# Kernel tuning notes

Hardware: AMD Instinct MI355X
Metric: run time of the kernel (lower is better)

The kernel has to match this reference:

```python
import jax, jax.numpy as jnp
import numpy as np

HIDDEN = 1024
N_HEADS = 16
N_LAYERS = 10
LOCAL_K = 3
TOKEN_T, TOKEN_H, TOKEN_W = 4, 16, 16
PATCH_SIZE = 2
LATENT_C = 16
TOKEN_DIM = LATENT_C * PATCH_SIZE * PATCH_SIZE  # 64
TOKEN_IN = TOKEN_DIM + 1                        # 65
N_TOKENS = TOKEN_T * TOKEN_H * TOKEN_W          # 1024
B = 1
HEAD_DIM = HIDDEN // N_HEADS
LN_EPS = 1e-5


def layer_norm(x, w, b):
    m = x.mean(-1, keepdims=True)
    v = ((x - m) ** 2).mean(-1, keepdims=True)
    return (x - m) * jax.lax.rsqrt(v + LN_EPS) * w + b


def patchify(lat):
    Bx, T, C, H, W = lat.shape
    ph, pw = H // PATCH_SIZE, W // PATCH_SIZE
    x = lat.reshape(Bx, T, C, ph, PATCH_SIZE, pw, PATCH_SIZE)
    x = x.transpose(0, 1, 3, 5, 2, 4, 6)
    return x.reshape(Bx, T * ph * pw, C * PATCH_SIZE * PATCH_SIZE)


def unpatchify(tok):
    Bx = tok.shape[0]
    C = TOKEN_DIM // (PATCH_SIZE * PATCH_SIZE)
    x = tok.reshape(Bx, TOKEN_T, TOKEN_H, TOKEN_W, C, PATCH_SIZE, PATCH_SIZE)
    x = x.transpose(0, 1, 4, 2, 5, 3, 6)
    return x.reshape(Bx, TOKEN_T, C, TOKEN_H * PATCH_SIZE, TOKEN_W * PATCH_SIZE)


def gather_neighbors(kv):
    # kv: (B, N, 2D) -> (B, N, 27, 2D), 3x3x3 zero-padded neighborhoods
    Bx, Nx, D2 = kv.shape
    pad = LOCAL_K // 2
    x = kv.reshape(Bx, TOKEN_T, TOKEN_H, TOKEN_W, D2)
    x = jnp.pad(x, ((0, 0), (pad, pad), (pad, pad), (pad, pad), (0, 0)))
    sl = [x[:, dt:dt + TOKEN_T, dh:dh + TOKEN_H, dw:dw + TOKEN_W]
          for dt in range(LOCAL_K) for dh in range(LOCAL_K) for dw in range(LOCAL_K)]
    nb = jnp.stack(sl, axis=4)  # (B,T,H,W,27,2D)
    return nb.reshape(Bx, Nx, LOCAL_K ** 3, D2)


def local_attention(x, qkv_w, out_w):
    Bx, Nx, D = x.shape
    H, d = N_HEADS, HEAD_DIM
    qkv = x @ qkv_w                       # (B,N,3D)
    q, k, v = jnp.split(qkv, 3, axis=-1)
    kv_nb = gather_neighbors(jnp.concatenate([k, v], axis=-1))  # (B,N,27,2D)
    k_nb, v_nb = jnp.split(kv_nb, 2, axis=-1)
    q = q.reshape(Bx, Nx, H, d)
    k_nb = k_nb.reshape(Bx, Nx, LOCAL_K ** 3, H, d)
    v_nb = v_nb.reshape(Bx, Nx, LOCAL_K ** 3, H, d)
    scores = jnp.einsum('bnhd,bnkhd->bnhk', q, k_nb) / np.sqrt(d).astype(np.float32)
    probs = jax.nn.softmax(scores, axis=-1)
    out = jnp.einsum('bnhk,bnkhd->bnhd', probs, v_nb).reshape(Bx, Nx, D)
    return out @ out_w


def global_attention(x, mask_flat, qkv_w, out_w):
    # Each masked query attends to all N keys; math identical to the
    # gather/SDPA/scatter in the original (per-query attention is independent),
    # realized as full attention masked to zero at unmasked positions.
    Bx, Nx, D = x.shape
    H, d = N_HEADS, HEAD_DIM
    qkv = x @ qkv_w
    q, k, v = jnp.split(qkv, 3, axis=-1)
    q = q.reshape(Bx, Nx, H, d)
    k = k.reshape(Bx, Nx, H, d)
    v = v.reshape(Bx, Nx, H, d)
    scores = jnp.einsum('bqhd,bkhd->bhqk', q, k) / np.sqrt(d).astype(np.float32)
    probs = jax.nn.softmax(scores, axis=-1)
    out = jnp.einsum('bhqk,bkhd->bqhd', probs, v).reshape(Bx, Nx, D)
    out = out @ out_w
    return out * mask_flat[..., None].astype(out.dtype)


def setup_inputs() -> dict:
    key = jax.random.key(0)
    ks = jax.random.split(key, 24)
    s = 0.02
    L, D = N_LAYERS, HIDDEN
    inp = {
        'latents': jax.random.normal(ks[0], (B, TOKEN_T, LATENT_C, TOKEN_H * PATCH_SIZE, TOKEN_W * PATCH_SIZE), jnp.float32),
        'token_mask': jax.random.uniform(ks[1], (B, TOKEN_T, TOKEN_H, TOKEN_W)) < 0.1,
        'input_proj_w': jax.random.normal(ks[2], (TOKEN_IN, D), jnp.float32) * s,
        'input_proj_b': jnp.zeros((D,), jnp.float32),
        'emb_t': jax.random.normal(ks[3], (TOKEN_T, D), jnp.float32) * s,
        'emb_h': jax.random.normal(ks[4], (TOKEN_H, D), jnp.float32) * s,
        'emb_w': jax.random.normal(ks[5], (TOKEN_W, D), jnp.float32) * s,
        'ln_local_w': jnp.ones((L, D), jnp.float32),
        'ln_local_b': jnp.zeros((L, D), jnp.float32),
        'ln_global_w': jnp.ones((L, D), jnp.float32),
        'ln_global_b': jnp.zeros((L, D), jnp.float32),
        'ln_ffn_w': jnp.ones((L, D), jnp.float32),
        'ln_ffn_b': jnp.zeros((L, D), jnp.float32),
        'local_qkv_w': jax.random.normal(ks[6], (L, D, 3 * D), jnp.float32) * s,
        'local_out_w': jax.random.normal(ks[7], (L, D, D), jnp.float32) * s,
        'global_qkv_w': jax.random.normal(ks[8], (L, D, 3 * D), jnp.float32) * s,
        'global_out_w': jax.random.normal(ks[9], (L, D, D), jnp.float32) * s,
        'ffn_w1': jax.random.normal(ks[10], (L, D, 4 * D), jnp.float32) * s,
        'ffn_b1': jnp.zeros((L, 4 * D), jnp.float32),
        'ffn_w2': jax.random.normal(ks[11], (L, 4 * D, D), jnp.float32) * s,
        'ffn_b2': jnp.zeros((L, D), jnp.float32),
        'final_ln_w': jnp.ones((D,), jnp.float32),
        'final_ln_b': jnp.zeros((D,), jnp.float32),
        # original zero-inits output_proj; use small random so the test is non-trivial
        'out_proj_w': jax.random.normal(ks[12], (D, TOKEN_DIM), jnp.float32) * s,
        'out_proj_b': jnp.zeros((TOKEN_DIM,), jnp.float32),
    }
    return inp


def reference(latents, token_mask, input_proj_w, input_proj_b, emb_t, emb_h, emb_w,
              ln_local_w, ln_local_b, ln_global_w, ln_global_b, ln_ffn_w, ln_ffn_b,
              local_qkv_w, local_out_w, global_qkv_w, global_out_w,
              ffn_w1, ffn_b1, ffn_w2, ffn_b2, final_ln_w, final_ln_b,
              out_proj_w, out_proj_b):
    Bx = latents.shape[0]
    mask_flat = token_mask.reshape(Bx, -1)
    tokens = patchify(latents)                       # (B, N, TOKEN_DIM)
    flag = mask_flat[..., None].astype(tokens.dtype)
    x = jnp.concatenate([tokens, flag], axis=-1) @ input_proj_w + input_proj_b

    tt, hh, ww = jnp.meshgrid(jnp.arange(TOKEN_T), jnp.arange(TOKEN_H), jnp.arange(TOKEN_W), indexing='ij')
    pos = emb_t[tt.reshape(-1)] + emb_h[hh.reshape(-1)] + emb_w[ww.reshape(-1)]
    x = x + pos[None]

    for l in range(N_LAYERS):
        x = x + local_attention(layer_norm(x, ln_local_w[l], ln_local_b[l]), local_qkv_w[l], local_out_w[l])
        x = x + global_attention(layer_norm(x, ln_global_w[l], ln_global_b[l]), mask_flat, global_qkv_w[l], global_out_w[l])
        h = layer_norm(x, ln_ffn_w[l], ln_ffn_b[l])
        h = jax.nn.gelu(h @ ffn_w1[l] + ffn_b1[l], approximate=False) @ ffn_w2[l] + ffn_b2[l]
        x = x + h

    delta = layer_norm(x, final_ln_w, final_ln_b) @ out_proj_w + out_proj_b
    return unpatchify(tokens + delta)
```

## Files before the change

kernel.cpp:

```cpp
#include <hip/hip_runtime.h>
#include <hip/hip_bf16.h>
#include <math.h>

typedef __bf16 bf16;
typedef __bf16 bf16x8 __attribute__((ext_vector_type(8)));
typedef __bf16 bf16x4 __attribute__((ext_vector_type(4)));
typedef float  f32x4 __attribute__((ext_vector_type(4)));
typedef unsigned int u32x4 __attribute__((ext_vector_type(4)));

#define NTOK 1024
#define HID  1024
#define NL   10
#define QCMAX 256

#define EPI_F32   0
#define EPI_GELU  1
#define EPI_RESID 2
#define EPI_BF16  3

__global__ __launch_bounds__(256)
void wtransall_k(const float* __restrict__ lqkv, const float* __restrict__ lout,
                 const float* __restrict__ gqkv, const float* __restrict__ gout,
                 const float* __restrict__ w1,   const float* __restrict__ w2,
                 bf16* __restrict__ lqkvT, bf16* __restrict__ loutT,
                 bf16* __restrict__ gqkvT, bf16* __restrict__ goutT,
                 bf16* __restrict__ w1T,   bf16* __restrict__ w2T)
{
    __shared__ bf16 tile[64 * 64];
    const int b = blockIdx.x;
    const float* W; bf16* O; int K, N, ti;
    if      (b < 768)  { W = lqkv; O = lqkvT; K = 1024; N = 3072; ti = b; }
    else if (b < 1024) { W = lout; O = loutT; K = 1024; N = 1024; ti = b - 768; }
    else if (b < 1792) { W = gqkv; O = gqkvT; K = 1024; N = 3072; ti = b - 1024; }
    else if (b < 2048) { W = gout; O = goutT; K = 1024; N = 1024; ti = b - 1792; }
    else if (b < 3072) { W = w1;   O = w1T;   K = 1024; N = 4096; ti = b - 2048; }
    else               { W = w2;   O = w2T;   K = 4096; N = 1024; ti = b - 3072; }
    const int ntx = N >> 6;
    const int n0 = (ti % ntx) * 64, k0 = (ti / ntx) * 64;
    const long mofs = (long)blockIdx.z * K * N;
    const float* Ws = W + mofs;
    bf16* Wo = O + mofs;
    const int t = threadIdx.x;
    {
        const int r = t >> 2, cc = (t & 3) * 16;
        const int x = (r >> 3) & 7;
        const int g0 = cc >> 3;
        const float* src = Ws + (long)(k0 + r) * N + n0 + cc;
        f32x4 a0 = *(const f32x4*)(src);
        f32x4 a1 = *(const f32x4*)(src + 4);
        f32x4 a2 = *(const f32x4*)(src + 8);
        f32x4 a3 = *(const f32x4*)(src + 12);
        bf16x8 w0, w1v;
        w0[0]=(bf16)a0.x; w0[1]=(bf16)a0.y; w0[2]=(bf16)a0.z; w0[3]=(bf16)a0.w;
        w0[4]=(bf16)a1.x; w0[5]=(bf16)a1.y; w0[6]=(bf16)a1.z; w0[7]=(bf16)a1.w;
        w1v[0]=(bf16)a2.x; w1v[1]=(bf16)a2.y; w1v[2]=(bf16)a2.z; w1v[3]=(bf16)a2.w;
        w1v[4]=(bf16)a3.x; w1v[5]=(bf16)a3.y; w1v[6]=(bf16)a3.z; w1v[7]=(bf16)a3.w;
        *(bf16x8*)&tile[r * 64 + ((g0    ) ^ x) * 8] = w0;
        *(bf16x8*)&tile[r * 64 + ((g0 | 1) ^ x) * 8] = w1v;
    }
    __syncthreads();
    {
        const int n = t >> 2, kc = (t & 3) * 16;
        const int g = n >> 3, no = n & 7;
        bf16x8 o0, o1;
#pragma unroll
        for (int j = 0; j < 8; ++j) {
            int r0 = kc + j, r1 = kc + 8 + j;
            o0[j] = tile[r0 * 64 + ((g ^ ((r0 >> 3) & 7)) * 8) + no];
            o1[j] = tile[r1 * 64 + ((g ^ ((r1 >> 3) & 7)) * 8) + no];
        }
        bf16* dst = Wo + (long)(n0 + n) * K + k0 + kc;
        *(bf16x8*)dst = o0;
        *(bf16x8*)(dst + 8) = o1;
    }
}

template<int EPI, int BM, int BN, int KSPLIT>
__global__ __launch_bounds__(256)
void gemm_k(const bf16* __restrict__ A, int lda, long bsA,
            const bf16* __restrict__ Bt, int ldb, long bsB,
            void* __restrict__ Cv, int ldc, long bsC,
            const float* __restrict__ bias, int K)
{
    constexpr int WC  = (BM == 128) ? 2 : 4;
    constexpr int WTN = BN / WC;
    constexpr int NF  = WTN / 16;
    constexpr int NLD = BM / 64 + BN / 64;
    __shared__ bf16 Al[2][BM * 32];
    __shared__ bf16 Bl[2][BN * 32];

    const int t    = threadIdx.x;
    const int lane = t & 63;
    const int wv   = t >> 6;
    const int wr   = wv / WC, wc = wv % WC;
    const int lrow = lane & 15, lk = lane >> 4;
    const int n0   = blockIdx.x * BN;
    const int m0   = blockIdx.y * BM;
    const int ks   = (KSPLIT > 1) ? (blockIdx.z % KSPLIT) : 0;
    const int bz   = (KSPLIT > 1) ? (blockIdx.z / KSPLIT) : blockIdx.z;
    const int Kc   = K / KSPLIT;

    const bf16* Ab = A  + bsA * bz + (long)ks * Kc;
    const bf16* Bb = Bt + bsB * bz + (long)ks * Kc;

    f32x4 acc[4][NF];
#pragma unroll
    for (int m = 0; m < 4; ++m)
#pragma unroll
        for (int n = 0; n < NF; ++n) acc[m][n] = f32x4{0.f, 0.f, 0.f, 0.f};

    const int sr = t >> 2, sc = (t & 3) * 8;

    auto stage = [&](int buf, int kk) {
#pragma unroll
        for (int i = 0; i < BM / 64; ++i)
            __builtin_amdgcn_global_load_lds(
                (const __attribute__((address_space(1))) void*)(Ab + (long)(m0 + sr + i * 64) * lda + kk + sc),
                (__attribute__((address_space(3))) void*)(&Al[buf][i * 2048 + t * 8]), 16, 0, 0);
#pragma unroll
        for (int i = 0; i < BN / 64; ++i)
            __builtin_amdgcn_global_load_lds(
                (const __attribute__((address_space(1))) void*)(Bb + (long)(n0 + sr + i * 64) * ldb + kk + sc),
                (__attribute__((address_space(3))) void*)(&Bl[buf][i * 2048 + t * 8]), 16, 0, 0);
    };

    const int nsteps = Kc >> 5;
    stage(0, 0);
    if (nsteps > 1) stage(1, 32);
    int cur = 0;
    for (int i = 0; i < nsteps; ++i) {
        if (i + 1 < nsteps) {
            if constexpr (NLD == 2)      asm volatile("s_waitcnt vmcnt(2)" ::: "memory");
            else if constexpr (NLD == 3) asm volatile("s_waitcnt vmcnt(3)" ::: "memory");
            else                         asm volatile("s_waitcnt vmcnt(4)" ::: "memory");
        } else {
            asm volatile("s_waitcnt vmcnt(0)" ::: "memory");
        }
        __builtin_amdgcn_s_barrier();

        bf16x8 af[4], bfv[NF];
#pragma unroll
        for (int m = 0; m < 4; ++m)
            af[m] = *(const bf16x8*)&Al[cur][(wr * 64 + m * 16 + lrow) * 32 + lk * 8];
#pragma unroll
        for (int n = 0; n < NF; ++n)
            bfv[n] = *(const bf16x8*)&Bl[cur][(wc * WTN + n * 16 + lrow) * 32 + lk * 8];
#pragma unroll
        for (int m = 0; m < 4; ++m)
#pragma unroll
            for (int n = 0; n < NF; ++n)
                acc[m][n] = __builtin_amdgcn_mfma_f32_16x16x32_bf16(af[m], bfv[n], acc[m][n], 0, 0, 0);

        __builtin_amdgcn_s_barrier();
        if (i + 2 < nsteps) stage(cur, (i + 2) * 32);
        cur ^= 1;
    }

    float* Cf = (float*)Cv + bsC * blockIdx.z;
    bf16*  Cb = (bf16*)Cv + bsC * blockIdx.z;
#pragma unroll
    for (int m = 0; m < 4; ++m)
#pragma unroll
        for (int n = 0; n < NF; ++n) {
            const int c = n0 + wc * WTN + n * 16 + lrow;
#pragma unroll
            for (int q = 0; q < 4; ++q) {
                const int r = m0 + wr * 64 + m * 16 + lk * 4 + q;
                const float v = acc[m][n][q];
                const long off = (long)r * ldc + c;
                if (EPI == EPI_F32)        Cf[off] = v;
                else if (EPI == EPI_BF16)  Cb[off] = (bf16)v;
                else if (EPI == EPI_RESID) Cf[off] += v;
                else {
                    float u = v + bias[c];
                    Cb[off] = (bf16)(0.5f * u * (1.f + erff(u * 0.70710678118654752f)));
                }
            }
        }
}

template<int NS, bool BIAS, bool SCATTER>
__global__ __launch_bounds__(256)
void ln_add_k(float* __restrict__ x, const float* __restrict__ parts, long pstride,
              const float* __restrict__ bias, const int* __restrict__ rmap,
              const float* __restrict__ w, const float* __restrict__ b,
              bf16* __restrict__ o)
{
    int row  = blockIdx.x * 4 + (threadIdx.x >> 6);
    int lane = threadIdx.x & 63;
    f32x4* xr = (f32x4*)(x + (long)row * HID) + lane * 4;
    f32x4 v[4];
#pragma unroll
    for (int i = 0; i < 4; ++i) v[i] = xr[i];

    if (NS > 0) {
        int prow = SCATTER ? rmap[row] : row;
        if (!SCATTER || prow >= 0) {
            const float* pp = parts + (long)prow * 1024 + lane * 16;
#pragma unroll
            for (int ksi = 0; ksi < NS; ++ksi) {
                const f32x4* q = (const f32x4*)(pp + (long)ksi * pstride);
#pragma unroll
                for (int i = 0; i < 4; ++i) v[i] += q[i];
            }
            if (BIAS) {
                const f32x4* bb = (const f32x4*)bias + lane * 4;
#pragma unroll
                for (int i = 0; i < 4; ++i) v[i] += bb[i];
            }
#pragma unroll
            for (int i = 0; i < 4; ++i) xr[i] = v[i];
        }
    }

    float s = 0.f;
#pragma unroll
    for (int i = 0; i < 4; ++i) s += v[i].x + v[i].y + v[i].z + v[i].w;
    for (int m = 32; m; m >>= 1) s += __shfl_xor(s, m);
    float mean = s * (1.f / 1024.f);
    f32x4 d[4];
    float ss = 0.f;
#pragma unroll
    for (int i = 0; i < 4; ++i) {
        d[i] = v[i] - mean;
        ss += d[i].x * d[i].x + d[i].y * d[i].y + d[i].z * d[i].z + d[i].w * d[i].w;
    }
    for (int m = 32; m; m >>= 1) ss += __shfl_xor(ss, m);
    float rs = rsqrtf(ss * (1.f / 1024.f) + 1e-5f);
    const f32x4* wp = (const f32x4*)w + lane * 4;
    const f32x4* bp = (const f32x4*)b + lane * 4;
    bf16x8 o0, o1;
#pragma unroll
    for (int i = 0; i < 4; ++i) {
        f32x4 wv = wp[i], bv = bp[i];
        f32x4 e;
        e.x = d[i].x * rs * wv.x + bv.x; e.y = d[i].y * rs * wv.y + bv.y;
        e.z = d[i].z * rs * wv.z + bv.z; e.w = d[i].w * rs * wv.w + bv.w;
        if (i < 2) { o0[i*4+0]=(bf16)e.x; o0[i*4+1]=(bf16)e.y; o0[i*4+2]=(bf16)e.z; o0[i*4+3]=(bf16)e.w; }
        else       { int k=(i-2)*4; o1[k+0]=(bf16)e.x; o1[k+1]=(bf16)e.y; o1[k+2]=(bf16)e.z; o1[k+3]=(bf16)e.w; }
    }
    bf16* op = o + (long)row * HID + lane * 16;
    *(bf16x8*)op = o0;
    *(bf16x8*)(op + 8) = o1;
}

__global__ __launch_bounds__(256)
void lattn_k(const bf16* __restrict__ qkv, bf16* __restrict__ ao)
{
    int w    = blockIdx.x * 4 + (threadIdx.x >> 6);
    int lane = threadIdx.x & 63;
    int n = w >> 4, h = w & 15;
    int tt = n >> 8, hh = (n >> 4) & 15, ww = n & 15;

    int nj = -1;
    float dotv = 0.f;
    if (lane < 27) {
        int dt = lane / 9 - 1, dh = (lane % 9) / 3 - 1, dw = lane % 3 - 1;
        int t2 = tt + dt, h2 = hh + dh, w2 = ww + dw;
        if (t2 >= 0 && t2 < 4 && h2 >= 0 && h2 < 16 && w2 >= 0 && w2 < 16)
            nj = (t2 << 8) | (h2 << 4) | w2;
    }
    if (nj >= 0) {
        const bf16x8* qp = (const bf16x8*)(qkv + (long)n * 3072 + h * 64);
        const bf16x8* kp = (const bf16x8*)(qkv + (long)nj * 3072 + 1024 + h * 64);
#pragma unroll
        for (int i = 0; i < 8; ++i) {
            bf16x8 q8 = qp[i], k8 = kp[i];
#pragma unroll
            for (int j = 0; j < 8; ++j) dotv += (float)q8[j] * (float)k8[j];
        }
    }
    float sc = (lane < 27) ? dotv * 0.125f : -3.0e38f;
    float mx = sc;
    for (int m = 32; m; m >>= 1) mx = fmaxf(mx, __shfl_xor(mx, m));
    float e = (lane < 27) ? __expf(sc - mx) : 0.f;
    float s = e;
    for (int m = 32; m; m >>= 1) s += __shfl_xor(s, m);
    float p = e / s;

    float acc = 0.f;
    for (int j = 0; j < 27; ++j) {
        float pj = __shfl(p, j);
        int  njj = __shfl(nj, j);
        if (njj >= 0) acc += pj * (float)qkv[(long)njj * 3072 + 2048 + h * 64 + lane];
    }
    ao[(long)n * 1024 + h * 64 + lane] = (bf16)acc;
}

__global__ void compact_k(const int* __restrict__ mask, int* __restrict__ qidx,
                          int* __restrict__ rmap)
{
    int lane = threadIdx.x;
    int total = 0;
    for (int base = 0; base < 1024; base += 64) {
        int m = (mask[base + lane] != 0) ? 1 : 0;
        unsigned long long bal = __ballot(m);
        int pos = total + (int)__popcll(bal & ((1ull << lane) - 1ull));
        int ok = (m && pos < QCMAX);
        if (ok) qidx[pos] = base + lane;
        rmap[base + lane] = ok ? pos : -1;
        total += (int)__popcll(bal);
    }
    for (int i = total + lane; i < QCMAX; i += 64) qidx[i] = -1;
}

__global__ __launch_bounds__(256)
void qkvbuild_k(const bf16* __restrict__ qkv, const int* __restrict__ qidx,
                bf16* __restrict__ Qc, bf16* __restrict__ Kh, bf16* __restrict__ Vt)
{
    __shared__ bf16 vt[64][72];
    const int h = blockIdx.y;
    const int t = threadIdx.x;
    if (blockIdx.x < 4) {
        const int r = blockIdx.x * 64 + (t >> 2), dc = (t & 3) * 16;
        const int q = qidx[r];
        bf16x8 o0, o1;
        if (q >= 0) {
            const bf16x8* src = (const bf16x8*)(qkv + (long)q * 3072 + h * 64 + dc);
            bf16x8 a = src[0], b = src[1];
#pragma unroll
            for (int j = 0; j < 8; ++j) {
                o0[j] = (bf16)((float)a[j] * 0.125f);
                o1[j] = (bf16)((float)b[j] * 0.125f);
            }
        } else {
#pragma unroll
            for (int j = 0; j < 8; ++j) { o0[j] = (bf16)0.f; o1[j] = (bf16)0.f; }
        }
        bf16* dst = Qc + (long)h * (QCMAX * 64) + (long)r * 64 + dc;
        *(bf16x8*)dst = o0;
        *(bf16x8*)(dst + 8) = o1;
        return;
    }
    const int k0 = (blockIdx.x - 4) * 64;
    {
        const int r = t >> 2, dc = (t & 3) * 16;
        const bf16x8* kp = (const bf16x8*)(qkv + (long)(k0 + r) * 3072 + 1024 + h * 64 + dc);
        const bf16x8* vp = (const bf16x8*)(qkv + (long)(k0 + r) * 3072 + 2048 + h * 64 + dc);
        bf16x8 k0v = kp[0], k1v = kp[1];
        bf16* kd = Kh + (long)h * (NTOK * 64) + (long)(k0 + r) * 64 + dc;
        *(bf16x8*)kd = k0v;
        *(bf16x8*)(kd + 8) = k1v;
        *(bf16x8*)&vt[r][dc]     = vp[0];
        *(bf16x8*)&vt[r][dc + 8] = vp[1];
    }
    __syncthreads();
    {
        const int d = t >> 2, kc = (t & 3) * 16;
        bf16x8 o0, o1;
#pragma unroll
        for (int j = 0; j < 8; ++j) { o0[j] = vt[kc + j][d]; o1[j] = vt[kc + 8 + j][d]; }
        bf16* dst = Vt + (long)h * (64 * NTOK) + (long)d * NTOK + k0 + kc;
        *(bf16x8*)dst = o0;
        *(bf16x8*)(dst + 8) = o1;
    }
}

__global__ __launch_bounds__(256)
void softmax_k(const float* __restrict__ S, bf16* __restrict__ P)
{
    int row  = blockIdx.x * 4 + (threadIdx.x >> 6);
    int lane = threadIdx.x & 63;
    const f32x4* sp = (const f32x4*)(S + (long)row * 1024) + lane * 4;
    f32x4 v[4];
#pragma unroll
    for (int i = 0; i < 4; ++i) v[i] = sp[i];
    float mx = -3.0e38f;
#pragma unroll
    for (int i = 0; i < 4; ++i)
        mx = fmaxf(mx, fmaxf(fmaxf(v[i].x, v[i].y), fmaxf(v[i].z, v[i].w)));
    for (int m = 32; m; m >>= 1) mx = fmaxf(mx, __shfl_xor(mx, m));
    f32x4 ev[4];
    float sum = 0.f;
#pragma unroll
    for (int i = 0; i < 4; ++i) {
        ev[i].x = __expf(v[i].x - mx); ev[i].y = __expf(v[i].y - mx);
        ev[i].z = __expf(v[i].z - mx); ev[i].w = __expf(v[i].w - mx);
        sum += ev[i].x + ev[i].y + ev[i].z + ev[i].w;
    }
    for (int m = 32; m; m >>= 1) sum += __shfl_xor(sum, m);
    float inv = 1.f / sum;
    bf16x8 o0, o1;
#pragma unroll
    for (int i = 0; i < 4; ++i) {
        f32x4 e = ev[i] * inv;
        if (i < 2) { o0[i*4+0]=(bf16)e.x; o0[i*4+1]=(bf16)e.y; o0[i*4+2]=(bf16)e.z; o0[i*4+3]=(bf16)e.w; }
        else       { int k=(i-2)*4; o1[k+0]=(bf16)e.x; o1[k+1]=(bf16)e.y; o1[k+2]=(bf16)e.z; o1[k+3]=(bf16)e.w; }
    }
    bf16* op = P + (long)row * 1024 + lane * 16;
    *(bf16x8*)op = o0;
    *(bf16x8*)(op + 8) = o1;
}

__global__ __launch_bounds__(256)
void prep_k(const float* __restrict__ lat, const int* __restrict__ mask,
            const float* __restrict__ Wi, const float* __restrict__ bi,
            const float* __restrict__ et, const float* __restrict__ eh,
            const float* __restrict__ ew,
            float* __restrict__ x, float* __restrict__ tokens)
{
    __shared__ float tl[16][65];
    int t = threadIdx.x;
    int n0 = blockIdx.x * 16;
    for (int idx = t; idx < 16 * 65; idx += 256) {
        int ti = idx / 65, d = idx % 65;
        int n = n0 + ti;
        int tt = n >> 8, hh = (n >> 4) & 15, wwi = n & 15;
        float v;
        if (d < 64) {
            int c = d >> 2, ph = (d >> 1) & 1, pw = d & 1;
            v = lat[(((long)tt * 16 + c) * 32 + hh * 2 + ph) * 32 + wwi * 2 + pw];
            tokens[(long)n * 64 + d] = v;
        } else {
            v = mask[n] ? 1.f : 0.f;
        }
        tl[ti][d] = v;
    }
    __syncthreads();
    f32x4 acc[16];
#pragma unroll
    for (int i = 0; i < 16; ++i) acc[i] = f32x4{0.f, 0.f, 0.f, 0.f};
    for (int d = 0; d < 65; ++d) {
        f32x4 wv = *(const f32x4*)(Wi + (long)d * 1024 + t * 4);
#pragma unroll
        for (int ti = 0; ti < 16; ++ti) acc[ti] += tl[ti][d] * wv;
    }
    f32x4 bb = *(const f32x4*)(bi + t * 4);
    for (int ti = 0; ti < 16; ++ti) {
        int n = n0 + ti;
        int tt = n >> 8, hh = (n >> 4) & 15, wwi = n & 15;
        f32x4 pos = *(const f32x4*)(et + (long)tt * 1024 + t * 4)
                  + *(const f32x4*)(eh + (long)hh * 1024 + t * 4)
                  + *(const f32x4*)(ew + (long)wwi * 1024 + t * 4);
        *(f32x4*)(x + (long)n * 1024 + t * 4) = acc[ti] + bb + pos;
    }
}

__global__ __launch_bounds__(256)
void final_k(const bf16* __restrict__ xn, const float* __restrict__ OW,
             const float* __restrict__ ob, const float* __restrict__ tokens,
             float* __restrict__ out)
{
    __shared__ bf16 xl[8][1024];
    __shared__ float part[4][8][64];
    int t = threadIdx.x;
    int n0 = blockIdx.x * 8;
    for (int i = t; i < 1024; i += 256)
        ((u32x4*)xl)[i] = ((const u32x4*)(xn + (long)n0 * 1024))[i];
    __syncthreads();
    int j = t & 63, s = t >> 6;
    float acc[8] = {0.f, 0.f, 0.f, 0.f, 0.f, 0.f, 0.f, 0.f};
    for (int k = s * 256; k < s * 256 + 256; ++k) {
        float w = OW[(long)k * 64 + j];
#pragma unroll
        for (int ti = 0; ti < 8; ++ti) acc[ti] += (float)xl[ti][k] * w;
    }
    for (int ti = 0; ti < 8; ++ti) part[s][ti][j] = acc[ti];
    __syncthreads();
    if (s == 0) {
        for (int ti = 0; ti < 8; ++ti) {
            int n = n0 + ti;
            float v = part[0][ti][j] + part[1][ti][j] + part[2][ti][j] + part[3][ti][j]
                    + ob[j] + tokens[(long)n * 64 + j];
            int tt = n >> 8, hh = (n >> 4) & 15, wwi = n & 15;
            int c = j >> 2, ph = (j >> 1) & 1, pw = j & 1;
            out[(((long)tt * 16 + c) * 32 + hh * 2 + ph) * 32 + wwi * 2 + pw] = v;
        }
    }
}

extern "C" void kernel_launch(void* const* d_in, const int* in_sizes, int n_in,
                              void* d_out, int out_size, void* d_ws, size_t ws_size,
                              hipStream_t stream)
{
    const float* latents = (const float*)d_in[0];
    const int*   mask    = (const int*)d_in[1];
    const float* ipw  = (const float*)d_in[2];
    const float* ipb  = (const float*)d_in[3];
    const float* et   = (const float*)d_in[4];
    const float* eh   = (const float*)d_in[5];
    const float* ew   = (const float*)d_in[6];
    const float* lnlw = (const float*)d_in[7];
    const float* lnlb = (const float*)d_in[8];
    const float* lngw = (const float*)d_in[9];
    const float* lngb = (const float*)d_in[10];
    const float* lnfw = (const float*)d_in[11];
    const float* lnfb = (const float*)d_in[12];
    const float* lqkv = (const float*)d_in[13];
    const float* lout = (const float*)d_in[14];
    const float* gqkv = (const float*)d_in[15];
    const float* gout = (const float*)d_in[16];
    const float* w1   = (const float*)d_in[17];
    const float* b1   = (const float*)d_in[18];
    const float* w2   = (const float*)d_in[19];
    const float* b2   = (const float*)d_in[20];
    const float* flw  = (const float*)d_in[21];
    const float* flb  = (const float*)d_in[22];
    const float* opw  = (const float*)d_in[23];
    const float* opb  = (const float*)d_in[24];

    char* p = (char*)d_ws;
    auto alloc = [&](size_t bytes) { char* r = p; p += (bytes + 255) & ~(size_t)255; return r; };
    float* x      = (float*)alloc((size_t)4 << 20);
    bf16*  xn     = (bf16*)alloc((size_t)2 << 20);
    bf16*  qkvb   = (bf16*)alloc((size_t)6 << 20);
    bf16*  ao     = (bf16*)alloc((size_t)2 << 20);
    bf16*  hbuf   = (bf16*)alloc((size_t)8 << 20);
    float* tokens = (float*)alloc((size_t)256 << 10);
    bf16*  Qc     = (bf16*)alloc((size_t)512 << 10);
    bf16*  Kh     = (bf16*)alloc((size_t)2 << 20);
    bf16*  Vt     = (bf16*)alloc((size_t)2 << 20);
    float* S      = (float*)alloc((size_t)16 << 20);
    bf16*  P      = (bf16*)alloc((size_t)8 << 20);
    bf16*  Oc     = (bf16*)alloc((size_t)512 << 10);
    int*   qidx   = (int*)alloc(4096);
    int*   rmap   = (int*)alloc(4096);
    float* goutp  = (float*)alloc((size_t)8 * 256 * 1024 * 4);
    float* f2p    = (float*)alloc((size_t)4 * 1024 * 1024 * 4);
    bf16* lqkvT = (bf16*)alloc((size_t)10 * 3072 * 1024 * 2);
    bf16* loutT = (bf16*)alloc((size_t)10 * 1024 * 1024 * 2);
    bf16* gqkvT = (bf16*)alloc((size_t)10 * 3072 * 1024 * 2);
    bf16* goutT = (bf16*)alloc((size_t)10 * 1024 * 1024 * 2);
    bf16* w1T   = (bf16*)alloc((size_t)10 * 4096 * 1024 * 2);
    bf16* w2T   = (bf16*)alloc((size_t)10 * 1024 * 4096 * 2);

    wtransall_k<<<dim3(4096, 1, NL), 256, 0, stream>>>(
        lqkv, lout, gqkv, gout, w1, w2, lqkvT, loutT, gqkvT, goutT, w1T, w2T);

    prep_k<<<64, 256, 0, stream>>>(latents, mask, ipw, ipb, et, eh, ew, x, tokens);
    compact_k<<<1, 64, 0, stream>>>(mask, qidx, rmap);

    for (int l = 0; l < NL; ++l) {
        const long wq  = (long)l * 3072 * 1024;
        const long wo  = (long)l * 1024 * 1024;
        const long wf1 = (long)l * 4096 * 1024;

        if (l == 0)
            ln_add_k<0, false, false><<<256, 256, 0, stream>>>(
                x, nullptr, 0, nullptr, nullptr, lnlw, lnlb, xn);
        else
            ln_add_k<4, true, false><<<256, 256, 0, stream>>>(
                x, f2p, (long)1024 * 1024, b2 + (l - 1) * 1024, nullptr,
                lnlw + l * HID, lnlb + l * HID, xn);

        gemm_k<EPI_BF16, 64, 128, 1><<<dim3(24, 16, 1), 256, 0, stream>>>(
            xn, 1024, 0, lqkvT + wq, 1024, 0, qkvb, 3072, 0, nullptr, 1024);
        lattn_k<<<4096, 256, 0, stream>>>(qkvb, ao);
        gemm_k<EPI_RESID, 64, 128, 1><<<dim3(8, 16, 1), 256, 0, stream>>>(
            ao, 1024, 0, loutT + wo, 1024, 0, x, 1024, 0, nullptr, 1024);

        ln_add_k<0, false, false><<<256, 256, 0, stream>>>(
            x, nullptr, 0, nullptr, nullptr, lngw + l * HID, lngb + l * HID, xn);

        gemm_k<EPI_BF16, 64, 128, 1><<<dim3(24, 16, 1), 256, 0, stream>>>(
            xn, 1024, 0, gqkvT + wq, 1024, 0, qkvb, 3072, 0, nullptr, 1024);
        qkvbuild_k<<<dim3(20, 16), 256, 0, stream>>>(qkvb, qidx, Qc, Kh, Vt);
        gemm_k<EPI_F32, 64, 128, 1><<<dim3(8, 4, 16), 256, 0, stream>>>(
            Qc, 64, (long)256 * 64, Kh, 64, (long)1024 * 64,
            S, 1024, (long)256 * 1024, nullptr, 64);
        softmax_k<<<1024, 256, 0, stream>>>(S, P);
        gemm_k<EPI_BF16, 64, 64, 1><<<dim3(1, 4, 16), 256, 0, stream>>>(
            P, 1024, (long)256 * 1024, Vt, 1024, (long)64 * 1024,
            Oc, 1024, 64, nullptr, 1024);
        gemm_k<EPI_F32, 64, 128, 8><<<dim3(8, 4, 8), 256, 0, stream>>>(
            Oc, 1024, 0, goutT + wo, 1024, 0, goutp, 1024, (long)256 * 1024, nullptr, 1024);

        ln_add_k<8, false, true><<<256, 256, 0, stream>>>(
            x, goutp, (long)256 * 1024, nullptr, rmap,
            lnfw + l * HID, lnfb + l * HID, xn);

        gemm_k<EPI_GELU, 64, 128, 1><<<dim3(32, 16, 1), 256, 0, stream>>>(
            xn, 1024, 0, w1T + wf1, 1024, 0, hbuf, 4096, 0, b1 + l * 4096, 1024);
        gemm_k<EPI_F32, 64, 128, 4><<<dim3(8, 16, 4), 256, 0, stream>>>(
            hbuf, 4096, 0, w2T + wf1, 4096, 0, f2p, 1024, (long)1024 * 1024, nullptr, 4096);
    }

    ln_add_k<4, true, false><<<256, 256, 0, stream>>>(
        x, f2p, (long)1024 * 1024, b2 + 9 * 1024, nullptr, flw, flb, xn);
    final_k<<<128, 256, 0, stream>>>(xn, opw, opb, tokens, (float*)d_out);
}
```

Baseline: 2.164 ms.

## Triple-buffer GEMM LDS staging and use 128x128 weight transpose tiles

The GEMM's K-loop moves from double to triple buffering of the global-to-LDS tiles, so each step prefetches three steps ahead, with vmcnt waits adjusted to the number of loads in flight. Separately, the weight fp32-to-bf16 transpose kernel now uses 128x128 tiles with a new XOR swizzle and a quarter as many blocks. The aim is to hide more global memory latency in the GEMMs and to cut block overhead in the transpose. The cost is more LDS per block (3 buffers, and 32KB in the transpose), which may lower occupancy.

```diff
diff --git a/kernel.cpp b/kernel.cpp
--- a/kernel.cpp
+++ b/kernel.cpp
@@ -26,52 +26,54 @@
                  bf16* __restrict__ gqkvT, bf16* __restrict__ goutT,
                  bf16* __restrict__ w1T,   bf16* __restrict__ w2T)
 {
-    __shared__ bf16 tile[64 * 64];
+    __shared__ bf16 tile[128 * 128];
     const int b = blockIdx.x;
     const float* W; bf16* O; int K, N, ti;
-    if      (b < 768)  { W = lqkv; O = lqkvT; K = 1024; N = 3072; ti = b; }
-    else if (b < 1024) { W = lout; O = loutT; K = 1024; N = 1024; ti = b - 768; }
-    else if (b < 1792) { W = gqkv; O = gqkvT; K = 1024; N = 3072; ti = b - 1024; }
-    else if (b < 2048) { W = gout; O = goutT; K = 1024; N = 1024; ti = b - 1792; }
-    else if (b < 3072) { W = w1;   O = w1T;   K = 1024; N = 4096; ti = b - 2048; }
-    else               { W = w2;   O = w2T;   K = 4096; N = 1024; ti = b - 3072; }
-    const int ntx = N >> 6;
-    const int n0 = (ti % ntx) * 64, k0 = (ti / ntx) * 64;
+    if      (b < 192)  { W = lqkv; O = lqkvT; K = 1024; N = 3072; ti = b; }
+    else if (b < 256)  { W = lout; O = loutT; K = 1024; N = 1024; ti = b - 192; }
+    else if (b < 448)  { W = gqkv; O = gqkvT; K = 1024; N = 3072; ti = b - 256; }
+    else if (b < 512)  { W = gout; O = goutT; K = 1024; N = 1024; ti = b - 448; }
+    else if (b < 768)  { W = w1;   O = w1T;   K = 1024; N = 4096; ti = b - 512; }
+    else               { W = w2;   O = w2T;   K = 4096; N = 1024; ti = b - 768; }
+    const int ntx = N >> 7;
+    const int n0 = (ti % ntx) * 128, k0 = (ti / ntx) * 128;
     const long mofs = (long)blockIdx.z * K * N;
     const float* Ws = W + mofs;
     bf16* Wo = O + mofs;
     const int t = threadIdx.x;
+
+#pragma unroll
+    for (int it = 0; it < 2; ++it) {
+        const int r = it * 64 + (t >> 2);
+        const int cc = (t & 3) * 32;
+        const float* src = Ws + (long)(k0 + r) * N + n0 + cc;
+#pragma unroll
+        for (int gp = 0; gp < 4; ++gp) {
+            f32x4 a = *(const f32x4*)(src + gp * 8);
+            f32x4 b4 = *(const f32x4*)(src + gp * 8 + 4);
+            bf16x8 w;
+            w[0]=(bf16)a.x;  w[1]=(bf16)a.y;  w[2]=(bf16)a.z;  w[3]=(bf16)a.w;
+            w[4]=(bf16)b4.x; w[5]=(bf16)b4.y; w[6]=(bf16)b4.z; w[7]=(bf16)b4.w;
+            const int g = (cc >> 3) + gp;
+            *(bf16x8*)&tile[r * 128 + ((g ^ (r & 15)) << 3)] = w;
+        }
+    }
+    __syncthreads();
+
     {
-        const int r = t >> 2, cc = (t & 3) * 16;
-        const int x = (r >> 3) & 7;
-        const int g0 = cc >> 3;
-        const float* src = Ws + (long)(k0 + r) * N + n0 + cc;
-        f32x4 a0 = *(const f32x4*)(src);
-        f32x4 a1 = *(const f32x4*)(src + 4);
-        f32x4 a2 = *(const f32x4*)(src + 8);
-        f32x4 a3 = *(const f32x4*)(src + 12);
-        bf16x8 w0, w1v;
-        w0[0]=(bf16)a0.x; w0[1]=(bf16)a0.y; w0[2]=(bf16)a0.z; w0[3]=(bf16)a0.w;
-        w0[4]=(bf16)a1.x; w0[5]=(bf16)a1.y; w0[6]=(bf16)a1.z; w0[7]=(bf16)a1.w;
-        w1v[0]=(bf16)a2.x; w1v[1]=(bf16)a2.y; w1v[2]=(bf16)a2.z; w1v[3]=(bf16)a2.w;
-        w1v[4]=(bf16)a3.x; w1v[5]=(bf16)a3.y; w1v[6]=(bf16)a3.z; w1v[7]=(bf16)a3.w;
-        *(bf16x8*)&tile[r * 64 + ((g0    ) ^ x) * 8] = w0;
-        *(bf16x8*)&tile[r * 64 + ((g0 | 1) ^ x) * 8] = w1v;
-    }
-    __syncthreads();
-    {
-        const int n = t >> 2, kc = (t & 3) * 16;
-        const int g = n >> 3, no = n & 7;
-        bf16x8 o0, o1;
-#pragma unroll
-        for (int j = 0; j < 8; ++j) {
-            int r0 = kc + j, r1 = kc + 8 + j;
-            o0[j] = tile[r0 * 64 + ((g ^ ((r0 >> 3) & 7)) * 8) + no];
-            o1[j] = tile[r1 * 64 + ((g ^ ((r1 >> 3) & 7)) * 8) + no];
-        }
+        const int n = t & 127, kc = (t >> 7) * 64;
+        const int gn = n >> 3, on = n & 7;
         bf16* dst = Wo + (long)(n0 + n) * K + k0 + kc;
-        *(bf16x8*)dst = o0;
-        *(bf16x8*)(dst + 8) = o1;
+#pragma unroll
+        for (int c = 0; c < 8; ++c) {
+            bf16x8 o;
+#pragma unroll
+            for (int j = 0; j < 8; ++j) {
+                const int k = kc + c * 8 + j;
+                o[j] = tile[k * 128 + ((gn ^ (k & 15)) << 3) + on];
+            }
+            *(bf16x8*)(dst + c * 8) = o;
+        }
     }
 }
 
@@ -86,8 +88,8 @@
     constexpr int WTN = BN / WC;
     constexpr int NF  = WTN / 16;
     constexpr int NLD = BM / 64 + BN / 64;
-    __shared__ bf16 Al[2][BM * 32];
-    __shared__ bf16 Bl[2][BN * 32];
+    __shared__ bf16 Al[3][BM * 32];
+    __shared__ bf16 Bl[3][BN * 32];
 
     const int t    = threadIdx.x;
     const int lane = t & 63;
@@ -127,9 +129,15 @@
     const int nsteps = Kc >> 5;
     stage(0, 0);
     if (nsteps > 1) stage(1, 32);
+    if (nsteps > 2) stage(2, 64);
     int cur = 0;
     for (int i = 0; i < nsteps; ++i) {
-        if (i + 1 < nsteps) {
+        const int rem = nsteps - 1 - i;
+        if (rem >= 2) {
+            if constexpr (NLD == 2)      asm volatile("s_waitcnt vmcnt(4)" ::: "memory");
+            else if constexpr (NLD == 3) asm volatile("s_waitcnt vmcnt(6)" ::: "memory");
+            else                         asm volatile("s_waitcnt vmcnt(8)" ::: "memory");
+        } else if (rem == 1) {
             if constexpr (NLD == 2)      asm volatile("s_waitcnt vmcnt(2)" ::: "memory");
             else if constexpr (NLD == 3) asm volatile("s_waitcnt vmcnt(3)" ::: "memory");
             else                         asm volatile("s_waitcnt vmcnt(4)" ::: "memory");
@@ -152,8 +160,8 @@
                 acc[m][n] = __builtin_amdgcn_mfma_f32_16x16x32_bf16(af[m], bfv[n], acc[m][n], 0, 0, 0);
 
         __builtin_amdgcn_s_barrier();
-        if (i + 2 < nsteps) stage(cur, (i + 2) * 32);
-        cur ^= 1;
+        if (i + 3 < nsteps) stage(cur, (i + 3) * 32);
+        cur = (cur == 2) ? 0 : cur + 1;
     }
 
     float* Cf = (float*)Cv + bsC * blockIdx.z;
@@ -524,7 +532,7 @@
     bf16* w1T   = (bf16*)alloc((size_t)10 * 4096 * 1024 * 2);
     bf16* w2T   = (bf16*)alloc((size_t)10 * 1024 * 4096 * 2);
 
-    wtransall_k<<<dim3(4096, 1, NL), 256, 0, stream>>>(
+    wtransall_k<<<dim3(1024, 1, NL), 256, 0, stream>>>(
         lqkv, lout, gqkv, gout, w1, w2, lqkvT, loutT, gqkvT, goutT, w1T, w2T);
 
     prep_k<<<64, 256, 0, stream>>>(latents, mask, ipw, ipb, et, eh, ew, x, tokens);
```

After: 2.181 ms. Within noise of the previous version (+0.8%).

## Fuse global softmax into PV via online softmax and gather Q rows in GEMM

Applied to the files above, without the earlier changes.

The global-attention path stops materializing Qc, Kh and the bf16 probability matrix P. The QK^T GEMM now reads Q rows indirectly through the compacted index map, and reads K straight from the qkv buffer using the row stride. A new single-wave pvfused_k kernel does an online (flash-style) softmax over the fp32 scores and accumulates P·V with MFMA. This removes the softmax kernel and the Q/K copy traffic. The cost is a small 256-block, 64-thread PV kernel with low occupancy and serial K iterations. The 1/8 scale moves from Q to the scores, and padded query rows now point at row 0 and are computed rather than zeroed.

```diff
diff --git a/kernel.cpp b/kernel.cpp
--- a/kernel.cpp
+++ b/kernel.cpp
@@ -75,13 +75,14 @@
     }
 }
 
-template<int EPI, int BM, int BN, int KSPLIT>
+template<int EPI, int BM, int BN, int KSPLIT, bool AIDX>
 __global__ __launch_bounds__(256)
 void gemm_k(const bf16* __restrict__ A, int lda, long bsA,
             const bf16* __restrict__ Bt, int ldb, long bsB,
             void* __restrict__ Cv, int ldc, long bsC,
-            const float* __restrict__ bias, int K)
-{
+            const float* __restrict__ bias, const int* __restrict__ qmap, int K)
+{
+    static_assert(!AIDX || BM == 64, "AIDX path assumes BM=64");
     constexpr int WC  = (BM == 128) ? 2 : 4;
     constexpr int WTN = BN / WC;
     constexpr int NF  = WTN / 16;
@@ -111,11 +112,22 @@
 
     const int sr = t >> 2, sc = (t & 3) * 8;
 
+    long arows[BM / 64];
+#pragma unroll
+    for (int i = 0; i < BM / 64; ++i) {
+        if (AIDX) {
+            int qv = qmap[m0 + sr + i * 64];
+            arows[i] = (qv < 0) ? 0 : qv;
+        } else {
+            arows[i] = m0 + sr + i * 64;
+        }
+    }
+
     auto stage = [&](int buf, int kk) {
 #pragma unroll
         for (int i = 0; i < BM / 64; ++i)
             __builtin_amdgcn_global_load_lds(
-                (const __attribute__((address_space(1))) void*)(Ab + (long)(m0 + sr + i * 64) * lda + kk + sc),
+                (const __attribute__((address_space(1))) void*)(Ab + arows[i] * lda + kk + sc),
                 (__attribute__((address_space(3))) void*)(&Al[buf][i * 2048 + t * 8]), 16, 0, 0);
 #pragma unroll
         for (int i = 0; i < BN / 64; ++i)
@@ -179,6 +191,68 @@
         }
 }
 
+__global__ __launch_bounds__(64)
+void pvfused_k(const float* __restrict__ S, const bf16* __restrict__ Vt,
+               bf16* __restrict__ Oc)
+{
+    const int lane = threadIdx.x;
+    const int lrow = lane & 15, lk = lane >> 4;
+    const int h = blockIdx.y;
+    const int q0 = blockIdx.x * 16;
+
+    const float* sp = S + (long)h * (QCMAX * 1024) + (long)(q0 + lrow) * 1024 + lk * 8;
+    const bf16*  vb = Vt + (long)h * (64 * NTOK);
+
+    f32x4 oacc[4];
+#pragma unroll
+    for (int nf = 0; nf < 4; ++nf) oacc[nf] = f32x4{0.f, 0.f, 0.f, 0.f};
+    float m = -3.0e38f, l = 0.f;
+
+    for (int k0 = 0; k0 < NTOK; k0 += 32) {
+        f32x4 s0 = *(const f32x4*)(sp + k0) * 0.125f;
+        f32x4 s1 = *(const f32x4*)(sp + k0 + 4) * 0.125f;
+        float cm = fmaxf(fmaxf(fmaxf(s0.x, s0.y), fmaxf(s0.z, s0.w)),
+                         fmaxf(fmaxf(s1.x, s1.y), fmaxf(s1.z, s1.w)));
+        cm = fmaxf(cm, __shfl_xor(cm, 16));
+        cm = fmaxf(cm, __shfl_xor(cm, 32));
+        float mn = fmaxf(m, cm);
+        float scl = __expf(m - mn);
+        m = mn;
+        float p[8];
+        p[0] = __expf(s0.x - mn); p[1] = __expf(s0.y - mn);
+        p[2] = __expf(s0.z - mn); p[3] = __expf(s0.w - mn);
+        p[4] = __expf(s1.x - mn); p[5] = __expf(s1.y - mn);
+        p[6] = __expf(s1.z - mn); p[7] = __expf(s1.w - mn);
+        float ls = p[0] + p[1] + p[2] + p[3] + p[4] + p[5] + p[6] + p[7];
+        ls += __shfl_xor(ls, 16);
+        ls += __shfl_xor(ls, 32);
+        l = l * scl + ls;
+#pragma unroll
+        for (int qi = 0; qi < 4; ++qi) {
+            float so = __shfl(scl, lk * 4 + qi);
+#pragma unroll
+            for (int nf = 0; nf < 4; ++nf) oacc[nf][qi] *= so;
+        }
+        bf16x8 pa;
+#pragma unroll
+        for (int j = 0; j < 8; ++j) pa[j] = (bf16)p[j];
+#pragma unroll
+        for (int nf = 0; nf < 4; ++nf) {
+            bf16x8 vv = *(const bf16x8*)(vb + (long)(nf * 16 + lrow) * NTOK + k0 + lk * 8);
+            oacc[nf] = __builtin_amdgcn_mfma_f32_16x16x32_bf16(pa, vv, oacc[nf], 0, 0, 0);
+        }
+    }
+
+#pragma unroll
+    for (int qi = 0; qi < 4; ++qi) {
+        float linv = 1.f / __shfl(l, lk * 4 + qi);
+        const int q = q0 + lk * 4 + qi;
+#pragma unroll
+        for (int nf = 0; nf < 4; ++nf)
+            Oc[(long)q * 1024 + h * 64 + nf * 16 + lrow] = (bf16)(oacc[nf][qi] * linv);
+    }
+}
+
 template<int NS, bool BIAS, bool SCATTER>
 __global__ __launch_bounds__(256)
 void ln_add_k(float* __restrict__ x, const float* __restrict__ parts, long pstride,
@@ -305,42 +379,15 @@
 }
 
 __global__ __launch_bounds__(256)
-void qkvbuild_k(const bf16* __restrict__ qkv, const int* __restrict__ qidx,
-                bf16* __restrict__ Qc, bf16* __restrict__ Kh, bf16* __restrict__ Vt)
+void vtbuild_k(const bf16* __restrict__ qkv, bf16* __restrict__ Vt)
 {
     __shared__ bf16 vt[64][72];
     const int h = blockIdx.y;
     const int t = threadIdx.x;
-    if (blockIdx.x < 4) {
-        const int r = blockIdx.x * 64 + (t >> 2), dc = (t & 3) * 16;
-        const int q = qidx[r];
-        bf16x8 o0, o1;
-        if (q >= 0) {
-            const bf16x8* src = (const bf16x8*)(qkv + (long)q * 3072 + h * 64 + dc);
-            bf16x8 a = src[0], b = src[1];
-#pragma unroll
-            for (int j = 0; j < 8; ++j) {
-                o0[j] = (bf16)((float)a[j] * 0.125f);
-                o1[j] = (bf16)((float)b[j] * 0.125f);
-            }
-        } else {
-#pragma unroll
-            for (int j = 0; j < 8; ++j) { o0[j] = (bf16)0.f; o1[j] = (bf16)0.f; }
-        }
-        bf16* dst = Qc + (long)h * (QCMAX * 64) + (long)r * 64 + dc;
-        *(bf16x8*)dst = o0;
-        *(bf16x8*)(dst + 8) = o1;
-        return;
-    }
-    const int k0 = (blockIdx.x - 4) * 64;
+    const int k0 = blockIdx.x * 64;
     {
         const int r = t >> 2, dc = (t & 3) * 16;
-        const bf16x8* kp = (const bf16x8*)(qkv + (long)(k0 + r) * 3072 + 1024 + h * 64 + dc);
         const bf16x8* vp = (const bf16x8*)(qkv + (long)(k0 + r) * 3072 + 2048 + h * 64 + dc);
-        bf16x8 k0v = kp[0], k1v = kp[1];
-        bf16* kd = Kh + (long)h * (NTOK * 64) + (long)(k0 + r) * 64 + dc;
-        *(bf16x8*)kd = k0v;
-        *(bf16x8*)(kd + 8) = k1v;
         *(bf16x8*)&vt[r][dc]     = vp[0];
         *(bf16x8*)&vt[r][dc + 8] = vp[1];
     }
@@ -354,42 +401,6 @@
         *(bf16x8*)dst = o0;
         *(bf16x8*)(dst + 8) = o1;
     }
-}
-
-__global__ __launch_bounds__(256)
-void softmax_k(const float* __restrict__ S, bf16* __restrict__ P)
-{
-    int row  = blockIdx.x * 4 + (threadIdx.x >> 6);
-    int lane = threadIdx.x & 63;
-    const f32x4* sp = (const f32x4*)(S + (long)row * 1024) + lane * 4;
-    f32x4 v[4];
-#pragma unroll
-    for (int i = 0; i < 4; ++i) v[i] = sp[i];
-    float mx = -3.0e38f;
-#pragma unroll
-    for (int i = 0; i < 4; ++i)
-        mx = fmaxf(mx, fmaxf(fmaxf(v[i].x, v[i].y), fmaxf(v[i].z, v[i].w)));
-    for (int m = 32; m; m >>= 1) mx = fmaxf(mx, __shfl_xor(mx, m));
-    f32x4 ev[4];
-    float sum = 0.f;
-#pragma unroll
-    for (int i = 0; i < 4; ++i) {
-        ev[i].x = __expf(v[i].x - mx); ev[i].y = __expf(v[i].y - mx);
-        ev[i].z = __expf(v[i].z - mx); ev[i].w = __expf(v[i].w - mx);
-        sum += ev[i].x + ev[i].y + ev[i].z + ev[i].w;
-    }
-    for (int m = 32; m; m >>= 1) sum += __shfl_xor(sum, m);
-    float inv = 1.f / sum;
-    bf16x8 o0, o1;
-#pragma unroll
-    for (int i = 0; i < 4; ++i) {
-        f32x4 e = ev[i] * inv;
-        if (i < 2) { o0[i*4+0]=(bf16)e.x; o0[i*4+1]=(bf16)e.y; o0[i*4+2]=(bf16)e.z; o0[i*4+3]=(bf16)e.w; }
-        else       { int k=(i-2)*4; o1[k+0]=(bf16)e.x; o1[k+1]=(bf16)e.y; o1[k+2]=(bf16)e.z; o1[k+3]=(bf16)e.w; }
-    }
-    bf16* op = P + (long)row * 1024 + lane * 16;
-    *(bf16x8*)op = o0;
-    *(bf16x8*)(op + 8) = o1;
 }
 
 __global__ __launch_bounds__(256)
@@ -507,11 +518,8 @@
     bf16*  ao     = (bf16*)alloc((size_t)2 << 20);
     bf16*  hbuf   = (bf16*)alloc((size_t)8 << 20);
     float* tokens = (float*)alloc((size_t)256 << 10);
-    bf16*  Qc     = (bf16*)alloc((size_t)512 << 10);
-    bf16*  Kh     = (bf16*)alloc((size_t)2 << 20);
     bf16*  Vt     = (bf16*)alloc((size_t)2 << 20);
     float* S      = (float*)alloc((size_t)16 << 20);
-    bf16*  P      = (bf16*)alloc((size_t)8 << 20);
     bf16*  Oc     = (bf16*)alloc((size_t)512 << 10);
     int*   qidx   = (int*)alloc(4096);
     int*   rmap   = (int*)alloc(4096);
@@ -543,36 +551,33 @@
                 x, f2p, (long)1024 * 1024, b2 + (l - 1) * 1024, nullptr,
                 lnlw + l * HID, lnlb + l * HID, xn);
 
-        gemm_k<EPI_BF16, 64, 128, 1><<<dim3(24, 16, 1), 256, 0, stream>>>(
-            xn, 1024, 0, lqkvT + wq, 1024, 0, qkvb, 3072, 0, nullptr, 1024);
+        gemm_k<EPI_BF16, 64, 128, 1, false><<<dim3(24, 16, 1), 256, 0, stream>>>(
+            xn, 1024, 0, lqkvT + wq, 1024, 0, qkvb, 3072, 0, nullptr, nullptr, 1024);
         lattn_k<<<4096, 256, 0, stream>>>(qkvb, ao);
-        gemm_k<EPI_RESID, 64, 128, 1><<<dim3(8, 16, 1), 256, 0, stream>>>(
-            ao, 1024, 0, loutT + wo, 1024, 0, x, 1024, 0, nullptr, 1024);
+        gemm_k<EPI_RESID, 64, 128, 1, false><<<dim3(8, 16, 1), 256, 0, stream>>>(
+            ao, 1024, 0, loutT + wo, 1024, 0, x, 1024, 0, nullptr, nullptr, 1024);
 
         ln_add_k<0, false, false><<<256, 256, 0, stream>>>(
             x, nullptr, 0, nullptr, nullptr, lngw + l * HID, lngb + l * HID, xn);
 
-        gemm_k<EPI_BF16, 64, 128, 1><<<dim3(24, 16, 1), 256, 0, stream>>>(
-            xn, 1024, 0, gqkvT + wq, 1024, 0, qkvb, 3072, 0, nullptr, 1024);
-        qkvbuild_k<<<dim3(20, 16), 256, 0, stream>>>(qkvb, qidx, Qc, Kh, Vt);
-        gemm_k<EPI_F32, 64, 128, 1><<<dim3(8, 4, 16), 256, 0, stream>>>(
-            Qc, 64, (long)256 * 64, Kh, 64, (long)1024 * 64,
-            S, 1024, (long)256 * 1024, nullptr, 64);
-        softmax_k<<<1024, 256, 0, stream>>>(S, P);
-        gemm_k<EPI_BF16, 64, 64, 1><<<dim3(1, 4, 16), 256, 0, stream>>>(
-            P, 1024, (long)256 * 1024, Vt, 1024, (long)64 * 1024,
-            Oc, 1024, 64, nullptr, 1024);
-        gemm_k<EPI_F32, 64, 128, 8><<<dim3(8, 4, 8), 256, 0, stream>>>(
-            Oc, 1024, 0, goutT + wo, 1024, 0, goutp, 1024, (long)256 * 1024, nullptr, 1024);
+        gemm_k<EPI_BF16, 64, 128, 1, false><<<dim3(24, 16, 1), 256, 0, stream>>>(
+            xn, 1024, 0, gqkvT + wq, 1024, 0, qkvb, 3072, 0, nullptr, nullptr, 1024);
+        vtbuild_k<<<dim3(16, 16), 256, 0, stream>>>(qkvb, Vt);
+        gemm_k<EPI_F32, 64, 128, 1, true><<<dim3(8, 4, 16), 256, 0, stream>>>(
+            qkvb, 3072, 64, qkvb + 1024, 3072, 64,
+            S, 1024, (long)256 * 1024, nullptr, qidx, 64);
+        pvfused_k<<<dim3(16, 16), 64, 0, stream>>>(S, Vt, Oc);
+        gemm_k<EPI_F32, 64, 128, 8, false><<<dim3(8, 4, 8), 256, 0, stream>>>(
+            Oc, 1024, 0, goutT + wo, 1024, 0, goutp, 1024, (long)256 * 1024, nullptr, nullptr, 1024);
 
         ln_add_k<8, false, true><<<256, 256, 0, stream>>>(
             x, goutp, (long)256 * 1024, nullptr, rmap,
             lnfw + l * HID, lnfb + l * HID, xn);
 
-        gemm_k<EPI_GELU, 64, 128, 1><<<dim3(32, 16, 1), 256, 0, stream>>>(
-            xn, 1024, 0, w1T + wf1, 1024, 0, hbuf, 4096, 0, b1 + l * 4096, 1024);
-        gemm_k<EPI_F32, 64, 128, 4><<<dim3(8, 16, 4), 256, 0, stream>>>(
-            hbuf, 4096, 0, w2T + wf1, 4096, 0, f2p, 1024, (long)1024 * 1024, nullptr, 4096);
+        gemm_k<EPI_GELU, 64, 128, 1, false><<<dim3(32, 16, 1), 256, 0, stream>>>(
+            xn, 1024, 0, w1T + wf1, 1024, 0, hbuf, 4096, 0, b1 + l * 4096, nullptr, 1024);
+        gemm_k<EPI_F32, 64, 128, 4, false><<<dim3(8, 16, 4), 256, 0, stream>>>(
+            hbuf, 4096, 0, w2T + wf1, 4096, 0, f2p, 1024, (long)1024 * 1024, nullptr, nullptr, 4096);
     }
 
     ln_add_k<4, true, false><<<256, 256, 0, stream>>>(
```

New measurement: 2.196 ms. No clear change (+1.5%).
